# Kernel tuning notes

Measured on AMD Instinct MI355X. Metric: run time of the kernel, lower is better.

The kernel has to match this reference:

```python
import jax, jax.numpy as jnp
import numpy as np
import math

EMB = 768
B, S = 8, 2048

def setup_inputs() -> dict:
    key = jax.random.key(0)
    ks = jax.random.split(key, 6)
    q = jax.random.normal(ks[0], (B, S, EMB), dtype=jnp.float32)
    k = jax.random.normal(ks[1], (B, S, EMB), dtype=jnp.float32)
    v = jax.random.normal(ks[2], (B, S, EMB), dtype=jnp.float32)
    mask = jax.random.randint(ks[3], (B, S, S), 0, 2, dtype=jnp.int32)
    # nn.Linear(emb, emb): weight [out, in], bias [out]
    bound = 1.0 / math.sqrt(EMB)
    W = jax.random.uniform(ks[4], (EMB, EMB), minval=-bound, maxval=bound, dtype=jnp.float32)
    b = jax.random.uniform(ks[5], (EMB,), minval=-bound, maxval=bound, dtype=jnp.float32)
    return {"q": q, "k": k, "v": v, "mask": mask, "W": W, "b": b}

def reference(q, k, v, mask, W, b):
    # shared linear projection (torch Linear: x @ W^T + b)
    qp = jnp.einsum('bse,oe->bso', q, W) + b
    kp = jnp.einsum('bse,oe->bso', k, W) + b
    vp = jnp.einsum('bse,oe->bso', v, W) + b
    scores = jnp.einsum('bqe,bke->bqk', qp, kp) / math.sqrt(EMB)  # [B,S,S]
    scores = jnp.where(mask == 1, -jnp.inf, scores)
    attn = jax.nn.softmax(scores, axis=-1)
    return jnp.einsum('bqk,bke->bqe', attn, vp)
```

## Files before the change

### kernel.cpp

```cpp
#include <hip/hip_runtime.h>
#include <hip/hip_bf16.h>
#include <stdint.h>

#define B_ 8
#define S_ 2048
#define E_ 768

typedef __attribute__((ext_vector_type(4))) float f32x4;
typedef __attribute__((ext_vector_type(8))) short bf16x8;


__device__ __forceinline__ unsigned pk2bf(float x, float y) {
  unsigned r;
  asm("v_cvt_pk_bf16_f32 %0, %1, %2" : "=v"(r) : "v"(x), "v"(y));
  return r;
}

__device__ __forceinline__ void gll16(const void* g, void* l) {
  __builtin_amdgcn_global_load_lds((const __attribute__((address_space(1))) void*)g,
                                   (__attribute__((address_space(3))) void*)l, 16, 0, 0);
}

__device__ __forceinline__ void gemm128(const char* __restrict__ Ab,
                                        const char* __restrict__ Bb,
                                        int ldA, int ldB, int NT,
                                        unsigned short* As, unsigned short* Bs,
                                        int tid, int wm, int wn, int lane,
                                        f32x4 (&acc)[4][4]) {
  unsigned sA[2], sB[2], lin2[2];
#pragma unroll
  for (int i = 0; i < 2; ++i) {
    const unsigned lin = (unsigned)i * 4096u + (unsigned)tid * 16u;
    const unsigned row = lin >> 6, ch = (lin >> 4) & 3u;
    const unsigned sw = (ch ^ ((row >> 1) & 3u)) << 4;
    sA[i] = row * (unsigned)ldA + sw;
    sB[i] = row * (unsigned)ldB + sw;
    lin2[i] = lin;
  }
  unsigned aoff[4], boff[4];
#pragma unroll
  for (int m = 0; m < 4; ++m) {
    unsigned row = (unsigned)(wm * 64 + m * 16 + (lane & 15));
    aoff[m] = row * 64 + ((((unsigned)lane >> 4) ^ ((row >> 1) & 3u)) << 4);
    row = (unsigned)(wn * 64 + m * 16 + (lane & 15));
    boff[m] = row * 64 + ((((unsigned)lane >> 4) ^ ((row >> 1) & 3u)) << 4);
  }
#pragma unroll
  for (int i = 0; i < 2; ++i) {
    gll16(Ab + sA[i], (char*)As + lin2[i]);
    gll16(Bb + sB[i], (char*)Bs + lin2[i]);
  }
  asm volatile("s_waitcnt vmcnt(0)" ::: "memory");
  __builtin_amdgcn_s_barrier();
  __builtin_amdgcn_sched_barrier(0);
  for (int kt = 0; kt < NT; ++kt) {
    const char* Ac = (const char*)As + (kt & 1) * 8192;
    const char* Bc = (const char*)Bs + (kt & 1) * 8192;
    char* An = (char*)As + ((kt + 1) & 1) * 8192;
    char* Bn = (char*)Bs + ((kt + 1) & 1) * 8192;
    if (kt + 1 < NT) {
      const size_t ko = (size_t)(kt + 1) * 64;
#pragma unroll
      for (int i = 0; i < 2; ++i) {
        gll16(Ab + sA[i] + ko, An + lin2[i]);
        gll16(Bb + sB[i] + ko, Bn + lin2[i]);
      }
    }
    bf16x8 af[4], bf[4];
#pragma unroll
    for (int m = 0; m < 4; ++m) af[m] = *reinterpret_cast<const bf16x8*>(Ac + aoff[m]);
#pragma unroll
    for (int n = 0; n < 4; ++n) bf[n] = *reinterpret_cast<const bf16x8*>(Bc + boff[n]);
    asm volatile("s_waitcnt lgkmcnt(0)" ::: "memory");
    __builtin_amdgcn_sched_barrier(0);
    __builtin_amdgcn_s_setprio(1);
#pragma unroll
    for (int m = 0; m < 4; ++m)
#pragma unroll
      for (int n = 0; n < 4; ++n)
        acc[m][n] = __builtin_amdgcn_mfma_f32_16x16x32_bf16(af[m], bf[n], acc[m][n], 0, 0, 0);
    __builtin_amdgcn_s_setprio(0);
    if (kt + 1 < NT) {
      asm volatile("s_waitcnt vmcnt(0)" ::: "memory");
      __builtin_amdgcn_s_barrier();
      __builtin_amdgcn_sched_barrier(0);
    }
  }
}

__global__ __launch_bounds__(256) void k_cvt(const float* __restrict__ q,
                                             const float* __restrict__ k,
                                             const float* __restrict__ v,
                                             const float* __restrict__ W,
                                             const int* __restrict__ mask,
                                             unsigned short* __restrict__ qb,
                                             unsigned short* __restrict__ kb,
                                             unsigned short* __restrict__ vb,
                                             unsigned short* __restrict__ Wb,
                                             unsigned long long* __restrict__ mwords) {
  const int y = blockIdx.y;
  if (y == 3) {
    const int nchunks = B_ * S_ * (S_ / 256);
    const int lane = threadIdx.x & 63;
    const int wave = (blockIdx.x * 256 + threadIdx.x) >> 6;
    const int nw = gridDim.x * 4;
    int c = wave;
    for (; c + 3 * nw < nchunks; c += 4 * nw) {
      int4 v0 = *reinterpret_cast<const int4*>(&mask[(size_t)c * 256 + lane * 4]);
      int4 v1 = *reinterpret_cast<const int4*>(&mask[(size_t)(c + nw) * 256 + lane * 4]);
      int4 v2 = *reinterpret_cast<const int4*>(&mask[(size_t)(c + 2 * nw) * 256 + lane * 4]);
      int4 v3 = *reinterpret_cast<const int4*>(&mask[(size_t)(c + 3 * nw) * 256 + lane * 4]);
      unsigned long long a0 = __ballot(v0.x == 1), a1 = __ballot(v0.y == 1);
      unsigned long long a2 = __ballot(v0.z == 1), a3 = __ballot(v0.w == 1);
      unsigned long long b0 = __ballot(v1.x == 1), b1 = __ballot(v1.y == 1);
      unsigned long long b2 = __ballot(v1.z == 1), b3 = __ballot(v1.w == 1);
      unsigned long long c0 = __ballot(v2.x == 1), c1 = __ballot(v2.y == 1);
      unsigned long long c2 = __ballot(v2.z == 1), c3 = __ballot(v2.w == 1);
      unsigned long long d0 = __ballot(v3.x == 1), d1 = __ballot(v3.y == 1);
      unsigned long long d2 = __ballot(v3.z == 1), d3 = __ballot(v3.w == 1);
      if (lane == 0) {
        *reinterpret_cast<ulonglong2*>(&mwords[(size_t)c * 4]) = make_ulonglong2(a0, a1);
        *reinterpret_cast<ulonglong2*>(&mwords[(size_t)c * 4 + 2]) = make_ulonglong2(a2, a3);
        *reinterpret_cast<ulonglong2*>(&mwords[(size_t)(c + nw) * 4]) = make_ulonglong2(b0, b1);
        *reinterpret_cast<ulonglong2*>(&mwords[(size_t)(c + nw) * 4 + 2]) = make_ulonglong2(b2, b3);
        *reinterpret_cast<ulonglong2*>(&mwords[(size_t)(c + 2 * nw) * 4]) = make_ulonglong2(c0, c1);
        *reinterpret_cast<ulonglong2*>(&mwords[(size_t)(c + 2 * nw) * 4 + 2]) = make_ulonglong2(c2, c3);
        *reinterpret_cast<ulonglong2*>(&mwords[(size_t)(c + 3 * nw) * 4]) = make_ulonglong2(d0, d1);
        *reinterpret_cast<ulonglong2*>(&mwords[(size_t)(c + 3 * nw) * 4 + 2]) = make_ulonglong2(d2, d3);
      }
    }
    for (; c < nchunks; c += nw) {
      int4 v0 = *reinterpret_cast<const int4*>(&mask[(size_t)c * 256 + lane * 4]);
      unsigned long long a0 = __ballot(v0.x == 1), a1 = __ballot(v0.y == 1);
      unsigned long long a2 = __ballot(v0.z == 1), a3 = __ballot(v0.w == 1);
      if (lane == 0) {
        *reinterpret_cast<ulonglong2*>(&mwords[(size_t)c * 4]) = make_ulonglong2(a0, a1);
        *reinterpret_cast<ulonglong2*>(&mwords[(size_t)c * 4 + 2]) = make_ulonglong2(a2, a3);
      }
    }
    return;
  }
  if (y == 4) {
    if (blockIdx.x < 288) {
      const int i0 = blockIdx.x * 512 + threadIdx.x;
      const float4* s4 = reinterpret_cast<const float4*>(W);
      uint2* d2 = reinterpret_cast<uint2*>(Wb);
      float4 f0 = s4[i0];
      float4 f1 = s4[i0 + 256];
      d2[i0]       = make_uint2(pk2bf(f0.x, f0.y), pk2bf(f0.z, f0.w));
      d2[i0 + 256] = make_uint2(pk2bf(f1.x, f1.y), pk2bf(f1.z, f1.w));
    }
    return;
  }
  const float* src = (y == 0) ? q : (y == 1) ? k : v;
  unsigned short* dst = (y == 0) ? qb : (y == 1) ? kb : vb;
  const int i0 = blockIdx.x * 512 + threadIdx.x;
  const float4* s4 = reinterpret_cast<const float4*>(src);
  uint2* d2 = reinterpret_cast<uint2*>(dst);
  float4 f0 = s4[i0];
  float4 f1 = s4[i0 + 256];
  d2[i0]       = make_uint2(pk2bf(f0.x, f0.y), pk2bf(f0.z, f0.w));
  d2[i0 + 256] = make_uint2(pk2bf(f1.x, f1.y), pk2bf(f1.z, f1.w));
}

__global__ __launch_bounds__(256, 4) void k_projb(const unsigned short* __restrict__ Xb,
                                                  const unsigned short* __restrict__ Wb,
                                                  const float* __restrict__ bias,
                                                  unsigned short* __restrict__ qp,
                                                  unsigned short* __restrict__ kp,
                                                  unsigned short* __restrict__ vpT) {
  __shared__ __attribute__((aligned(16))) unsigned short SM[16896];
  unsigned short* As = SM;
  unsigned short* Bs = SM + 8192;
  const int tid = threadIdx.x, lane = tid & 63, wid = tid >> 6;
  const int wm = wid >> 1, wn = wid & 1;
  const int id = blockIdx.x;
  const int swz = (id & 7) * 288 + (id >> 3);
  const int z = swz / 768;
  const int rem = swz - z * 768;
  const int r0 = (rem / 6) * 128, c0 = (rem % 6) * 128;
  const unsigned short* X = Xb + (size_t)z * (B_ * S_ * E_);

  f32x4 acc[4][4] = {};
  gemm128((const char*)(X + (size_t)r0 * E_), (const char*)(Wb + (size_t)c0 * E_),
          E_ * 2, E_ * 2, E_ / 32, As, Bs, tid, wm, wn, lane, acc);

  float bcol[4];
#pragma unroll
  for (int n = 0; n < 4; ++n) bcol[n] = bias[c0 + wn * 64 + n * 16 + (lane & 15)];

  if (z == 2) {
    __syncthreads();
#pragma unroll
    for (int m = 0; m < 4; ++m)
#pragma unroll
      for (int r = 0; r < 4; ++r) {
        const int row = wm * 64 + m * 16 + (lane >> 4) * 4 + r;
#pragma unroll
        for (int n = 0; n < 4; ++n) {
          const int col = wn * 64 + n * 16 + (lane & 15);
          SM[col * 132 + row] = (unsigned short)pk2bf(acc[m][n][r] + bcol[n], 0.f);
        }
      }
    __syncthreads();
    const int b = r0 >> 11;
    const int s0 = r0 & 2047;
#pragma unroll
    for (int i = 0; i < 16; ++i) {
      const int f = i * 256 + tid;
      const int e = f >> 5, su = f & 31;
      uint2 val = *reinterpret_cast<const uint2*>(&SM[e * 132 + su * 4]);
      *reinterpret_cast<uint2*>(&vpT[((size_t)b * E_ + c0 + e) * S_ + s0 + su * 4]) = val;
    }
    return;
  }

  unsigned short* O = (z == 0) ? qp : kp;
#pragma unroll
  for (int m = 0; m < 4; ++m)
#pragma unroll
    for (int r = 0; r < 4; ++r) {
      const int row = r0 + wm * 64 + m * 16 + (lane >> 4) * 4 + r;
#pragma unroll
      for (int n = 0; n < 4; ++n) {
        const int col = c0 + wn * 64 + n * 16 + (lane & 15);
        O[(size_t)row * E_ + col] = (unsigned short)pk2bf(acc[m][n][r] + bcol[n], 0.f);
      }
    }
}

__global__ __launch_bounds__(256, 4) void k_scores(const unsigned short* __restrict__ qp,
                                                   const unsigned short* __restrict__ kp,
                                                   const unsigned long long* __restrict__ mwords,
                                                   unsigned short* __restrict__ P,
                                                   float* __restrict__ rowsum) {
  __shared__ __attribute__((aligned(16))) unsigned short SM[16384];
  unsigned short* As = SM;
  unsigned short* Bs = SM + 8192;
  float* rlds = (float*)SM;
  const int tid = threadIdx.x, lane = tid & 63, wid = tid >> 6;
  const int wm = wid >> 1, wn = wid & 1;
  const int id = blockIdx.x;
  const int swz = (id & 7) * 256 + (id >> 3);
  const int b = swz >> 8;
  const int qt = (swz >> 4) & 15, yt = swz & 15;
  f32x4 acc[4][4] = {};
  gemm128((const char*)(qp + ((size_t)b * S_ + qt * 128) * E_),
          (const char*)(kp + ((size_t)b * S_ + yt * 128) * E_),
          E_ * 2, E_ * 2, E_ / 32, As, Bs, tid, wm, wn, lane, acc);
  __syncthreads();

  const float SC = (float)(1.4426950408889634 / 27.712812921102035);
#pragma unroll
  for (int m = 0; m < 4; ++m)
#pragma unroll
    for (int r = 0; r < 4; ++r) {
      const int rloc = wm * 64 + m * 16 + (lane >> 4) * 4 + r;
      const int grow = qt * 128 + rloc;
      const size_t rowoff = ((size_t)b * S_ + grow) * S_;
      const unsigned long long mw =
          mwords[(((size_t)b * S_ + grow) * 8 + (yt >> 1)) * 4 + (lane & 3)];
      const int shb = (yt & 1) * 32 + wn * 16 + ((lane & 15) >> 2);
      const int cbase = yt * 128 + wn * 64 + (lane & 15);
      float radd = 0.f;
#pragma unroll
      for (int n = 0; n < 4; ++n) {
        float pv = ((mw >> (shb + n * 4)) & 1ull)
                       ? 0.f
                       : __builtin_amdgcn_exp2f(acc[m][n][r] * SC);
        radd += pv;
        P[rowoff + cbase + n * 16] = (unsigned short)pk2bf(pv, 0.f);
      }
      float vsum = radd;
      vsum += __shfl_xor(vsum, 1);
      vsum += __shfl_xor(vsum, 2);
      vsum += __shfl_xor(vsum, 4);
      vsum += __shfl_xor(vsum, 8);
      if ((lane & 15) == 0) rlds[rloc * 2 + wn] = vsum;
    }
  __syncthreads();
  if (tid < 128) {
    rowsum[(size_t)yt * (B_ * S_) + (size_t)b * S_ + qt * 128 + tid] =
        rlds[tid * 2] + rlds[tid * 2 + 1];
  }
}

__global__ __launch_bounds__(256) void k_invrs(const float* __restrict__ rowsum,
                                               float* __restrict__ inv_rs) {
  int i = blockIdx.x * 256 + threadIdx.x;
  float t = 0.f;
#pragma unroll
  for (int g = 0; g < 16; ++g) t += rowsum[(size_t)g * (B_ * S_) + i];
  inv_rs[i] = 1.0f / t;
}

__global__ __launch_bounds__(256, 4) void k_pv(const unsigned short* __restrict__ P,
                                               const unsigned short* __restrict__ vpT,
                                               const float* __restrict__ inv_rs,
                                               float* __restrict__ out) {
  __shared__ __attribute__((aligned(16))) unsigned short SM[16384];
  unsigned short* As = SM;
  unsigned short* Bs = SM + 8192;
  const int tid = threadIdx.x, lane = tid & 63, wid = tid >> 6;
  const int wm = wid >> 1, wn = wid & 1;
  const int id = blockIdx.x;
  const int swz = (id & 7) * 96 + (id >> 3);
  const int b = swz / 96;
  const int rem = swz - b * 96;
  const int mt = rem / 6, et = rem % 6;
  f32x4 acc[4][4] = {};
  gemm128((const char*)(P + ((size_t)b * S_ + mt * 128) * S_),
          (const char*)(vpT + ((size_t)b * E_ + et * 128) * S_),
          S_ * 2, S_ * 2, S_ / 32, As, Bs, tid, wm, wn, lane, acc);

#pragma unroll
  for (int m = 0; m < 4; ++m)
#pragma unroll
    for (int r = 0; r < 4; ++r) {
      const int grow = mt * 128 + wm * 64 + m * 16 + (lane >> 4) * 4 + r;
      const float inv = inv_rs[b * S_ + grow];
#pragma unroll
      for (int n = 0; n < 4; ++n) {
        const int col = et * 128 + wn * 64 + n * 16 + (lane & 15);
        out[((size_t)b * S_ + grow) * E_ + col] = acc[m][n][r] * inv;
      }
    }
}

extern "C" void kernel_launch(void* const* d_in, const int* in_sizes, int n_in,
                              void* d_out, int out_size, void* d_ws, size_t ws_size,
                              hipStream_t stream) {
  const float* q = (const float*)d_in[0];
  const float* k = (const float*)d_in[1];
  const float* v = (const float*)d_in[2];
  const int* mask = (const int*)d_in[3];
  const float* W = (const float*)d_in[4];
  const float* bias = (const float*)d_in[5];
  float* out = (float*)d_out;
  char* ws = (char*)d_ws;

  unsigned short* qb = (unsigned short*)(ws + 0);
  unsigned short* kb = (unsigned short*)(ws + 25165824);
  unsigned short* vb = (unsigned short*)(ws + 50331648);
  unsigned short* Wb = (unsigned short*)(ws + 75497472);
  unsigned short* qp = (unsigned short*)(ws + 76677120);
  unsigned short* kp = (unsigned short*)(ws + 101842944);
  unsigned short* vpT = (unsigned short*)(ws + 127008768);
  unsigned short* P = (unsigned short*)(ws + 0);
  float* rowsum = (float*)(ws + 75497472);
  float* inv_rs = (float*)(ws + 76546048);
  unsigned long long* mwords =
      (unsigned long long*)((char*)d_out + 25165824);
  (void)in_sizes; (void)n_in; (void)out_size; (void)ws_size;

  dim3 blk(256, 1, 1);
  k_cvt<<<dim3(6144, 5, 1), blk, 0, stream>>>(q, k, v, W, mask, qb, kb, vb, Wb, mwords);
  k_projb<<<dim3(2304, 1, 1), blk, 0, stream>>>(qb, Wb, bias, qp, kp, vpT);
  k_scores<<<dim3(2048, 1, 1), blk, 0, stream>>>(qp, kp, mwords, P, rowsum);
  k_invrs<<<dim3(64, 1, 1), blk, 0, stream>>>(rowsum, inv_rs);
  k_pv<<<dim3(768, 1, 1), blk, 0, stream>>>(P, vpT, inv_rs, out);
}
```

Baseline: 287.2 us.

## Fuse fp32-to-bf16 activation conversion into projection GEMM A-operand loads

The projection GEMM now reads q/k/v directly as fp32 from global memory into registers, converts them to bf16 in-kernel, and writes the result into swizzled LDS. This removes the separate conversion pass, along with the bf16 copies it wrote to and read back from the workspace. The mask packing and W conversion are split into their own kernels. The trade-off is that the GEMM now reads twice the A bytes and its A operand goes through a register-staged path instead of direct global-to-LDS loads, which may reduce overlap in the main loop.

```diff
diff --git a/kernel.cpp b/kernel.cpp
--- a/kernel.cpp
+++ b/kernel.cpp
@@ -88,82 +88,153 @@
   }
 }
 
-__global__ __launch_bounds__(256) void k_cvt(const float* __restrict__ q,
-                                             const float* __restrict__ k,
-                                             const float* __restrict__ v,
-                                             const float* __restrict__ W,
-                                             const int* __restrict__ mask,
-                                             unsigned short* __restrict__ qb,
-                                             unsigned short* __restrict__ kb,
-                                             unsigned short* __restrict__ vb,
-                                             unsigned short* __restrict__ Wb,
-                                             unsigned long long* __restrict__ mwords) {
-  const int y = blockIdx.y;
-  if (y == 3) {
-    const int nchunks = B_ * S_ * (S_ / 256);
-    const int lane = threadIdx.x & 63;
-    const int wave = (blockIdx.x * 256 + threadIdx.x) >> 6;
-    const int nw = gridDim.x * 4;
-    int c = wave;
-    for (; c + 3 * nw < nchunks; c += 4 * nw) {
-      int4 v0 = *reinterpret_cast<const int4*>(&mask[(size_t)c * 256 + lane * 4]);
-      int4 v1 = *reinterpret_cast<const int4*>(&mask[(size_t)(c + nw) * 256 + lane * 4]);
-      int4 v2 = *reinterpret_cast<const int4*>(&mask[(size_t)(c + 2 * nw) * 256 + lane * 4]);
-      int4 v3 = *reinterpret_cast<const int4*>(&mask[(size_t)(c + 3 * nw) * 256 + lane * 4]);
-      unsigned long long a0 = __ballot(v0.x == 1), a1 = __ballot(v0.y == 1);
-      unsigned long long a2 = __ballot(v0.z == 1), a3 = __ballot(v0.w == 1);
-      unsigned long long b0 = __ballot(v1.x == 1), b1 = __ballot(v1.y == 1);
-      unsigned long long b2 = __ballot(v1.z == 1), b3 = __ballot(v1.w == 1);
-      unsigned long long c0 = __ballot(v2.x == 1), c1 = __ballot(v2.y == 1);
-      unsigned long long c2 = __ballot(v2.z == 1), c3 = __ballot(v2.w == 1);
-      unsigned long long d0 = __ballot(v3.x == 1), d1 = __ballot(v3.y == 1);
-      unsigned long long d2 = __ballot(v3.z == 1), d3 = __ballot(v3.w == 1);
-      if (lane == 0) {
-        *reinterpret_cast<ulonglong2*>(&mwords[(size_t)c * 4]) = make_ulonglong2(a0, a1);
-        *reinterpret_cast<ulonglong2*>(&mwords[(size_t)c * 4 + 2]) = make_ulonglong2(a2, a3);
-        *reinterpret_cast<ulonglong2*>(&mwords[(size_t)(c + nw) * 4]) = make_ulonglong2(b0, b1);
-        *reinterpret_cast<ulonglong2*>(&mwords[(size_t)(c + nw) * 4 + 2]) = make_ulonglong2(b2, b3);
-        *reinterpret_cast<ulonglong2*>(&mwords[(size_t)(c + 2 * nw) * 4]) = make_ulonglong2(c0, c1);
-        *reinterpret_cast<ulonglong2*>(&mwords[(size_t)(c + 2 * nw) * 4 + 2]) = make_ulonglong2(c2, c3);
-        *reinterpret_cast<ulonglong2*>(&mwords[(size_t)(c + 3 * nw) * 4]) = make_ulonglong2(d0, d1);
-        *reinterpret_cast<ulonglong2*>(&mwords[(size_t)(c + 3 * nw) * 4 + 2]) = make_ulonglong2(d2, d3);
-      }
-    }
-    for (; c < nchunks; c += nw) {
-      int4 v0 = *reinterpret_cast<const int4*>(&mask[(size_t)c * 256 + lane * 4]);
-      unsigned long long a0 = __ballot(v0.x == 1), a1 = __ballot(v0.y == 1);
-      unsigned long long a2 = __ballot(v0.z == 1), a3 = __ballot(v0.w == 1);
-      if (lane == 0) {
-        *reinterpret_cast<ulonglong2*>(&mwords[(size_t)c * 4]) = make_ulonglong2(a0, a1);
-        *reinterpret_cast<ulonglong2*>(&mwords[(size_t)c * 4 + 2]) = make_ulonglong2(a2, a3);
-      }
-    }
-    return;
-  }
-  if (y == 4) {
-    if (blockIdx.x < 288) {
-      const int i0 = blockIdx.x * 512 + threadIdx.x;
-      const float4* s4 = reinterpret_cast<const float4*>(W);
-      uint2* d2 = reinterpret_cast<uint2*>(Wb);
-      float4 f0 = s4[i0];
-      float4 f1 = s4[i0 + 256];
-      d2[i0]       = make_uint2(pk2bf(f0.x, f0.y), pk2bf(f0.z, f0.w));
-      d2[i0 + 256] = make_uint2(pk2bf(f1.x, f1.y), pk2bf(f1.z, f1.w));
-    }
-    return;
-  }
-  const float* src = (y == 0) ? q : (y == 1) ? k : v;
-  unsigned short* dst = (y == 0) ? qb : (y == 1) ? kb : vb;
+__device__ __forceinline__ void gemm128_f32A(const char* __restrict__ Af0, int ldAf,
+                                             const char* __restrict__ Bb, int ldB, int NT,
+                                             unsigned short* As, unsigned short* Bs,
+                                             int tid, int wm, int wn, int lane,
+                                             f32x4 (&acc)[4][4]) {
+  unsigned sB[2], lin2[2];
+#pragma unroll
+  for (int i = 0; i < 2; ++i) {
+    const unsigned lin = (unsigned)i * 4096u + (unsigned)tid * 16u;
+    const unsigned row = lin >> 6, ch = (lin >> 4) & 3u;
+    const unsigned sw = (ch ^ ((row >> 1) & 3u)) << 4;
+    sB[i] = row * (unsigned)ldB + sw;
+    lin2[i] = lin;
+  }
+  const int arow = tid >> 1;
+  const int ahalf = tid & 1;
+  const char* Afb = Af0 + (size_t)arow * ldAf + (size_t)ahalf * 64;
+  unsigned awoff[2];
+#pragma unroll
+  for (int c = 0; c < 2; ++c) {
+    const unsigned chunk = (unsigned)(ahalf * 2 + c);
+    awoff[c] = (unsigned)arow * 64 + ((chunk ^ (((unsigned)arow >> 1) & 3u)) << 4);
+  }
+  unsigned aoff[4], boff[4];
+#pragma unroll
+  for (int m = 0; m < 4; ++m) {
+    unsigned row = (unsigned)(wm * 64 + m * 16 + (lane & 15));
+    aoff[m] = row * 64 + ((((unsigned)lane >> 4) ^ ((row >> 1) & 3u)) << 4);
+    row = (unsigned)(wn * 64 + m * 16 + (lane & 15));
+    boff[m] = row * 64 + ((((unsigned)lane >> 4) ^ ((row >> 1) & 3u)) << 4);
+  }
+  float4 fa[4];
+#pragma unroll
+  for (int i = 0; i < 4; ++i) fa[i] = *reinterpret_cast<const float4*>(Afb + i * 16);
+#pragma unroll
+  for (int i = 0; i < 2; ++i) gll16(Bb + sB[i], (char*)Bs + lin2[i]);
+  asm volatile("s_waitcnt vmcnt(0)" ::: "memory");
+  {
+    uint4 w0 = make_uint4(pk2bf(fa[0].x, fa[0].y), pk2bf(fa[0].z, fa[0].w),
+                          pk2bf(fa[1].x, fa[1].y), pk2bf(fa[1].z, fa[1].w));
+    uint4 w1 = make_uint4(pk2bf(fa[2].x, fa[2].y), pk2bf(fa[2].z, fa[2].w),
+                          pk2bf(fa[3].x, fa[3].y), pk2bf(fa[3].z, fa[3].w));
+    *reinterpret_cast<uint4*>((char*)As + awoff[0]) = w0;
+    *reinterpret_cast<uint4*>((char*)As + awoff[1]) = w1;
+  }
+  asm volatile("s_waitcnt lgkmcnt(0)" ::: "memory");
+  __builtin_amdgcn_s_barrier();
+  __builtin_amdgcn_sched_barrier(0);
+  for (int kt = 0; kt < NT; ++kt) {
+    const char* Ac = (const char*)As + (kt & 1) * 8192;
+    const char* Bc = (const char*)Bs + (kt & 1) * 8192;
+    char* An = (char*)As + ((kt + 1) & 1) * 8192;
+    char* Bn = (char*)Bs + ((kt + 1) & 1) * 8192;
+    if (kt + 1 < NT) {
+      const size_t ko = (size_t)(kt + 1) * 128;
+#pragma unroll
+      for (int i = 0; i < 4; ++i)
+        fa[i] = *reinterpret_cast<const float4*>(Afb + ko + i * 16);
+#pragma unroll
+      for (int i = 0; i < 2; ++i)
+        gll16(Bb + sB[i] + (size_t)(kt + 1) * 64, Bn + lin2[i]);
+    }
+    bf16x8 af[4], bf[4];
+#pragma unroll
+    for (int m = 0; m < 4; ++m) af[m] = *reinterpret_cast<const bf16x8*>(Ac + aoff[m]);
+#pragma unroll
+    for (int n = 0; n < 4; ++n) bf[n] = *reinterpret_cast<const bf16x8*>(Bc + boff[n]);
+    asm volatile("s_waitcnt lgkmcnt(0)" ::: "memory");
+    __builtin_amdgcn_sched_barrier(0);
+    __builtin_amdgcn_s_setprio(1);
+#pragma unroll
+    for (int m = 0; m < 4; ++m)
+#pragma unroll
+      for (int n = 0; n < 4; ++n)
+        acc[m][n] = __builtin_amdgcn_mfma_f32_16x16x32_bf16(af[m], bf[n], acc[m][n], 0, 0, 0);
+    __builtin_amdgcn_s_setprio(0);
+    if (kt + 1 < NT) {
+      asm volatile("s_waitcnt vmcnt(0)" ::: "memory");
+      uint4 w0 = make_uint4(pk2bf(fa[0].x, fa[0].y), pk2bf(fa[0].z, fa[0].w),
+                            pk2bf(fa[1].x, fa[1].y), pk2bf(fa[1].z, fa[1].w));
+      uint4 w1 = make_uint4(pk2bf(fa[2].x, fa[2].y), pk2bf(fa[2].z, fa[2].w),
+                            pk2bf(fa[3].x, fa[3].y), pk2bf(fa[3].z, fa[3].w));
+      *reinterpret_cast<uint4*>(An + awoff[0]) = w0;
+      *reinterpret_cast<uint4*>(An + awoff[1]) = w1;
+      asm volatile("s_waitcnt lgkmcnt(0)" ::: "memory");
+      __builtin_amdgcn_s_barrier();
+      __builtin_amdgcn_sched_barrier(0);
+    }
+  }
+}
+
+__global__ __launch_bounds__(256) void k_cvtW(const float* __restrict__ W,
+                                              unsigned short* __restrict__ Wb) {
   const int i0 = blockIdx.x * 512 + threadIdx.x;
-  const float4* s4 = reinterpret_cast<const float4*>(src);
-  uint2* d2 = reinterpret_cast<uint2*>(dst);
+  const float4* s4 = reinterpret_cast<const float4*>(W);
+  uint2* d2 = reinterpret_cast<uint2*>(Wb);
   float4 f0 = s4[i0];
   float4 f1 = s4[i0 + 256];
   d2[i0]       = make_uint2(pk2bf(f0.x, f0.y), pk2bf(f0.z, f0.w));
   d2[i0 + 256] = make_uint2(pk2bf(f1.x, f1.y), pk2bf(f1.z, f1.w));
 }
 
-__global__ __launch_bounds__(256, 4) void k_projb(const unsigned short* __restrict__ Xb,
+__global__ __launch_bounds__(256) void k_pack(const int* __restrict__ mask,
+                                              unsigned long long* __restrict__ mwords) {
+  const int nchunks = B_ * S_ * (S_ / 256);
+  const int lane = threadIdx.x & 63;
+  const int wave = (blockIdx.x * 256 + threadIdx.x) >> 6;
+  const int nw = gridDim.x * 4;
+  int c = wave;
+  for (; c + 3 * nw < nchunks; c += 4 * nw) {
+    int4 v0 = *reinterpret_cast<const int4*>(&mask[(size_t)c * 256 + lane * 4]);
+    int4 v1 = *reinterpret_cast<const int4*>(&mask[(size_t)(c + nw) * 256 + lane * 4]);
+    int4 v2 = *reinterpret_cast<const int4*>(&mask[(size_t)(c + 2 * nw) * 256 + lane * 4]);
+    int4 v3 = *reinterpret_cast<const int4*>(&mask[(size_t)(c + 3 * nw) * 256 + lane * 4]);
+    unsigned long long a0 = __ballot(v0.x == 1), a1 = __ballot(v0.y == 1);
+    unsigned long long a2 = __ballot(v0.z == 1), a3 = __ballot(v0.w == 1);
+    unsigned long long b0 = __ballot(v1.x == 1), b1 = __ballot(v1.y == 1);
+    unsigned long long b2 = __ballot(v1.z == 1), b3 = __ballot(v1.w == 1);
+    unsigned long long c0 = __ballot(v2.x == 1), c1 = __ballot(v2.y == 1);
+    unsigned long long c2 = __ballot(v2.z == 1), c3 = __ballot(v2.w == 1);
+    unsigned long long d0 = __ballot(v3.x == 1), d1 = __ballot(v3.y == 1);
+    unsigned long long d2 = __ballot(v3.z == 1), d3 = __ballot(v3.w == 1);
+    if (lane == 0) {
+      *reinterpret_cast<ulonglong2*>(&mwords[(size_t)c * 4]) = make_ulonglong2(a0, a1);
+      *reinterpret_cast<ulonglong2*>(&mwords[(size_t)c * 4 + 2]) = make_ulonglong2(a2, a3);
+      *reinterpret_cast<ulonglong2*>(&mwords[(size_t)(c + nw) * 4]) = make_ulonglong2(b0, b1);
+      *reinterpret_cast<ulonglong2*>(&mwords[(size_t)(c + nw) * 4 + 2]) = make_ulonglong2(b2, b3);
+      *reinterpret_cast<ulonglong2*>(&mwords[(size_t)(c + 2 * nw) * 4]) = make_ulonglong2(c0, c1);
+      *reinterpret_cast<ulonglong2*>(&mwords[(size_t)(c + 2 * nw) * 4 + 2]) = make_ulonglong2(c2, c3);
+      *reinterpret_cast<ulonglong2*>(&mwords[(size_t)(c + 3 * nw) * 4]) = make_ulonglong2(d0, d1);
+      *reinterpret_cast<ulonglong2*>(&mwords[(size_t)(c + 3 * nw) * 4 + 2]) = make_ulonglong2(d2, d3);
+    }
+  }
+  for (; c < nchunks; c += nw) {
+    int4 v0 = *reinterpret_cast<const int4*>(&mask[(size_t)c * 256 + lane * 4]);
+    unsigned long long a0 = __ballot(v0.x == 1), a1 = __ballot(v0.y == 1);
+    unsigned long long a2 = __ballot(v0.z == 1), a3 = __ballot(v0.w == 1);
+    if (lane == 0) {
+      *reinterpret_cast<ulonglong2*>(&mwords[(size_t)c * 4]) = make_ulonglong2(a0, a1);
+      *reinterpret_cast<ulonglong2*>(&mwords[(size_t)c * 4 + 2]) = make_ulonglong2(a2, a3);
+    }
+  }
+}
+
+__global__ __launch_bounds__(256, 4) void k_projb(const float* __restrict__ q,
+                                                  const float* __restrict__ k,
+                                                  const float* __restrict__ v,
                                                   const unsigned short* __restrict__ Wb,
                                                   const float* __restrict__ bias,
                                                   unsigned short* __restrict__ qp,
@@ -179,11 +250,12 @@
   const int z = swz / 768;
   const int rem = swz - z * 768;
   const int r0 = (rem / 6) * 128, c0 = (rem % 6) * 128;
-  const unsigned short* X = Xb + (size_t)z * (B_ * S_ * E_);
+  const float* X = (z == 0) ? q : (z == 1) ? k : v;
 
   f32x4 acc[4][4] = {};
-  gemm128((const char*)(X + (size_t)r0 * E_), (const char*)(Wb + (size_t)c0 * E_),
-          E_ * 2, E_ * 2, E_ / 32, As, Bs, tid, wm, wn, lane, acc);
+  gemm128_f32A((const char*)(X + (size_t)r0 * E_), E_ * 4,
+               (const char*)(Wb + (size_t)c0 * E_), E_ * 2, E_ / 32,
+               As, Bs, tid, wm, wn, lane, acc);
 
   float bcol[4];
 #pragma unroll
@@ -339,9 +411,6 @@
   float* out = (float*)d_out;
   char* ws = (char*)d_ws;
 
-  unsigned short* qb = (unsigned short*)(ws + 0);
-  unsigned short* kb = (unsigned short*)(ws + 25165824);
-  unsigned short* vb = (unsigned short*)(ws + 50331648);
   unsigned short* Wb = (unsigned short*)(ws + 75497472);
   unsigned short* qp = (unsigned short*)(ws + 76677120);
   unsigned short* kp = (unsigned short*)(ws + 101842944);
@@ -354,8 +423,9 @@
   (void)in_sizes; (void)n_in; (void)out_size; (void)ws_size;
 
   dim3 blk(256, 1, 1);
-  k_cvt<<<dim3(6144, 5, 1), blk, 0, stream>>>(q, k, v, W, mask, qb, kb, vb, Wb, mwords);
-  k_projb<<<dim3(2304, 1, 1), blk, 0, stream>>>(qb, Wb, bias, qp, kp, vpT);
+  k_cvtW<<<dim3(288, 1, 1), blk, 0, stream>>>(W, Wb);
+  k_pack<<<dim3(6144, 1, 1), blk, 0, stream>>>(mask, mwords);
+  k_projb<<<dim3(2304, 1, 1), blk, 0, stream>>>(q, k, v, Wb, bias, qp, kp, vpT);
   k_scores<<<dim3(2048, 1, 1), blk, 0, stream>>>(qp, kp, mwords, P, rowsum);
   k_invrs<<<dim3(64, 1, 1), blk, 0, stream>>>(rowsum, inv_rs);
   k_pv<<<dim3(768, 1, 1), blk, 0, stream>>>(P, vpT, inv_rs, out);
```

Result: slower. 294.3 us (+2.5%).

## Split fused conversion kernel and use 128x64 tiles for PV GEMM

Applied to the files above, without the earlier changes.

Splits the fused multi-purpose conversion kernel into separate q/k/v cast, W cast and mask bit-pack kernels, with the mask pack launched on 2048 blocks instead of 6144. Adds a 128x64 tiled GEMM helper and switches the P·V kernel to it. The helper doubles the block count to 1536, cuts LDS per block, and raises launch bounds to 6 blocks per CU for better occupancy and load balance. In exchange, each block reuses less data per tile, so global traffic for P rises, and the extra launches add overhead.

```diff
diff --git a/kernel.cpp b/kernel.cpp
--- a/kernel.cpp
+++ b/kernel.cpp
@@ -88,72 +88,88 @@
   }
 }
 
-__global__ __launch_bounds__(256) void k_cvt(const float* __restrict__ q,
-                                             const float* __restrict__ k,
-                                             const float* __restrict__ v,
-                                             const float* __restrict__ W,
-                                             const int* __restrict__ mask,
-                                             unsigned short* __restrict__ qb,
-                                             unsigned short* __restrict__ kb,
-                                             unsigned short* __restrict__ vb,
-                                             unsigned short* __restrict__ Wb,
-                                             unsigned long long* __restrict__ mwords) {
-  const int y = blockIdx.y;
-  if (y == 3) {
-    const int nchunks = B_ * S_ * (S_ / 256);
-    const int lane = threadIdx.x & 63;
-    const int wave = (blockIdx.x * 256 + threadIdx.x) >> 6;
-    const int nw = gridDim.x * 4;
-    int c = wave;
-    for (; c + 3 * nw < nchunks; c += 4 * nw) {
-      int4 v0 = *reinterpret_cast<const int4*>(&mask[(size_t)c * 256 + lane * 4]);
-      int4 v1 = *reinterpret_cast<const int4*>(&mask[(size_t)(c + nw) * 256 + lane * 4]);
-      int4 v2 = *reinterpret_cast<const int4*>(&mask[(size_t)(c + 2 * nw) * 256 + lane * 4]);
-      int4 v3 = *reinterpret_cast<const int4*>(&mask[(size_t)(c + 3 * nw) * 256 + lane * 4]);
-      unsigned long long a0 = __ballot(v0.x == 1), a1 = __ballot(v0.y == 1);
-      unsigned long long a2 = __ballot(v0.z == 1), a3 = __ballot(v0.w == 1);
-      unsigned long long b0 = __ballot(v1.x == 1), b1 = __ballot(v1.y == 1);
-      unsigned long long b2 = __ballot(v1.z == 1), b3 = __ballot(v1.w == 1);
-      unsigned long long c0 = __ballot(v2.x == 1), c1 = __ballot(v2.y == 1);
-      unsigned long long c2 = __ballot(v2.z == 1), c3 = __ballot(v2.w == 1);
-      unsigned long long d0 = __ballot(v3.x == 1), d1 = __ballot(v3.y == 1);
-      unsigned long long d2 = __ballot(v3.z == 1), d3 = __ballot(v3.w == 1);
-      if (lane == 0) {
-        *reinterpret_cast<ulonglong2*>(&mwords[(size_t)c * 4]) = make_ulonglong2(a0, a1);
-        *reinterpret_cast<ulonglong2*>(&mwords[(size_t)c * 4 + 2]) = make_ulonglong2(a2, a3);
-        *reinterpret_cast<ulonglong2*>(&mwords[(size_t)(c + nw) * 4]) = make_ulonglong2(b0, b1);
-        *reinterpret_cast<ulonglong2*>(&mwords[(size_t)(c + nw) * 4 + 2]) = make_ulonglong2(b2, b3);
-        *reinterpret_cast<ulonglong2*>(&mwords[(size_t)(c + 2 * nw) * 4]) = make_ulonglong2(c0, c1);
-        *reinterpret_cast<ulonglong2*>(&mwords[(size_t)(c + 2 * nw) * 4 + 2]) = make_ulonglong2(c2, c3);
-        *reinterpret_cast<ulonglong2*>(&mwords[(size_t)(c + 3 * nw) * 4]) = make_ulonglong2(d0, d1);
-        *reinterpret_cast<ulonglong2*>(&mwords[(size_t)(c + 3 * nw) * 4 + 2]) = make_ulonglong2(d2, d3);
-      }
-    }
-    for (; c < nchunks; c += nw) {
-      int4 v0 = *reinterpret_cast<const int4*>(&mask[(size_t)c * 256 + lane * 4]);
-      unsigned long long a0 = __ballot(v0.x == 1), a1 = __ballot(v0.y == 1);
-      unsigned long long a2 = __ballot(v0.z == 1), a3 = __ballot(v0.w == 1);
-      if (lane == 0) {
-        *reinterpret_cast<ulonglong2*>(&mwords[(size_t)c * 4]) = make_ulonglong2(a0, a1);
-        *reinterpret_cast<ulonglong2*>(&mwords[(size_t)c * 4 + 2]) = make_ulonglong2(a2, a3);
-      }
-    }
-    return;
-  }
-  if (y == 4) {
-    if (blockIdx.x < 288) {
-      const int i0 = blockIdx.x * 512 + threadIdx.x;
-      const float4* s4 = reinterpret_cast<const float4*>(W);
-      uint2* d2 = reinterpret_cast<uint2*>(Wb);
-      float4 f0 = s4[i0];
-      float4 f1 = s4[i0 + 256];
-      d2[i0]       = make_uint2(pk2bf(f0.x, f0.y), pk2bf(f0.z, f0.w));
-      d2[i0 + 256] = make_uint2(pk2bf(f1.x, f1.y), pk2bf(f1.z, f1.w));
-    }
-    return;
-  }
-  const float* src = (y == 0) ? q : (y == 1) ? k : v;
-  unsigned short* dst = (y == 0) ? qb : (y == 1) ? kb : vb;
+__device__ __forceinline__ void gemm128x64(const char* __restrict__ Ab,
+                                           const char* __restrict__ Bb,
+                                           int ldA, int ldB, int NT,
+                                           unsigned short* As, unsigned short* Bs,
+                                           int tid, int wm, int wn, int lane,
+                                           f32x4 (&acc)[4][2]) {
+  unsigned sA[2], lin2[2];
+#pragma unroll
+  for (int i = 0; i < 2; ++i) {
+    const unsigned lin = (unsigned)i * 4096u + (unsigned)tid * 16u;
+    const unsigned row = lin >> 6, ch = (lin >> 4) & 3u;
+    const unsigned sw = (ch ^ ((row >> 1) & 3u)) << 4;
+    sA[i] = row * (unsigned)ldA + sw;
+    lin2[i] = lin;
+  }
+  unsigned sB0, linB;
+  {
+    const unsigned lin = (unsigned)tid * 16u;
+    const unsigned row = lin >> 6, ch = (lin >> 4) & 3u;
+    const unsigned sw = (ch ^ ((row >> 1) & 3u)) << 4;
+    sB0 = row * (unsigned)ldB + sw;
+    linB = lin;
+  }
+  unsigned aoff[4], boff[2];
+#pragma unroll
+  for (int m = 0; m < 4; ++m) {
+    unsigned row = (unsigned)(wm * 64 + m * 16 + (lane & 15));
+    aoff[m] = row * 64 + ((((unsigned)lane >> 4) ^ ((row >> 1) & 3u)) << 4);
+  }
+#pragma unroll
+  for (int j = 0; j < 2; ++j) {
+    unsigned row = (unsigned)(wn * 32 + j * 16 + (lane & 15));
+    boff[j] = row * 64 + ((((unsigned)lane >> 4) ^ ((row >> 1) & 3u)) << 4);
+  }
+#pragma unroll
+  for (int i = 0; i < 2; ++i) gll16(Ab + sA[i], (char*)As + lin2[i]);
+  gll16(Bb + sB0, (char*)Bs + linB);
+  asm volatile("s_waitcnt vmcnt(0)" ::: "memory");
+  __builtin_amdgcn_s_barrier();
+  __builtin_amdgcn_sched_barrier(0);
+  for (int kt = 0; kt < NT; ++kt) {
+    const char* Ac = (const char*)As + (kt & 1) * 8192;
+    const char* Bc = (const char*)Bs + (kt & 1) * 4096;
+    char* An = (char*)As + ((kt + 1) & 1) * 8192;
+    char* Bn = (char*)Bs + ((kt + 1) & 1) * 4096;
+    if (kt + 1 < NT) {
+      const size_t ko = (size_t)(kt + 1) * 64;
+#pragma unroll
+      for (int i = 0; i < 2; ++i) gll16(Ab + sA[i] + ko, An + lin2[i]);
+      gll16(Bb + sB0 + ko, Bn + linB);
+    }
+    bf16x8 af[4], bf[2];
+#pragma unroll
+    for (int m = 0; m < 4; ++m) af[m] = *reinterpret_cast<const bf16x8*>(Ac + aoff[m]);
+#pragma unroll
+    for (int j = 0; j < 2; ++j) bf[j] = *reinterpret_cast<const bf16x8*>(Bc + boff[j]);
+    asm volatile("s_waitcnt lgkmcnt(0)" ::: "memory");
+    __builtin_amdgcn_sched_barrier(0);
+    __builtin_amdgcn_s_setprio(1);
+#pragma unroll
+    for (int m = 0; m < 4; ++m)
+#pragma unroll
+      for (int j = 0; j < 2; ++j)
+        acc[m][j] = __builtin_amdgcn_mfma_f32_16x16x32_bf16(af[m], bf[j], acc[m][j], 0, 0, 0);
+    __builtin_amdgcn_s_setprio(0);
+    if (kt + 1 < NT) {
+      asm volatile("s_waitcnt vmcnt(0)" ::: "memory");
+      __builtin_amdgcn_s_barrier();
+      __builtin_amdgcn_sched_barrier(0);
+    }
+  }
+}
+
+__global__ __launch_bounds__(256) void k_cvt3(const float* __restrict__ q,
+                                              const float* __restrict__ k,
+                                              const float* __restrict__ v,
+                                              unsigned short* __restrict__ qb,
+                                              unsigned short* __restrict__ kb,
+                                              unsigned short* __restrict__ vb) {
+  const int z = blockIdx.y;
+  const float* src = (z == 0) ? q : (z == 1) ? k : v;
+  unsigned short* dst = (z == 0) ? qb : (z == 1) ? kb : vb;
   const int i0 = blockIdx.x * 512 + threadIdx.x;
   const float4* s4 = reinterpret_cast<const float4*>(src);
   uint2* d2 = reinterpret_cast<uint2*>(dst);
@@ -161,6 +177,59 @@
   float4 f1 = s4[i0 + 256];
   d2[i0]       = make_uint2(pk2bf(f0.x, f0.y), pk2bf(f0.z, f0.w));
   d2[i0 + 256] = make_uint2(pk2bf(f1.x, f1.y), pk2bf(f1.z, f1.w));
+}
+
+__global__ __launch_bounds__(256) void k_cvtW(const float* __restrict__ W,
+                                              unsigned short* __restrict__ Wb) {
+  const int i0 = blockIdx.x * 512 + threadIdx.x;
+  const float4* s4 = reinterpret_cast<const float4*>(W);
+  uint2* d2 = reinterpret_cast<uint2*>(Wb);
+  float4 f0 = s4[i0];
+  float4 f1 = s4[i0 + 256];
+  d2[i0]       = make_uint2(pk2bf(f0.x, f0.y), pk2bf(f0.z, f0.w));
+  d2[i0 + 256] = make_uint2(pk2bf(f1.x, f1.y), pk2bf(f1.z, f1.w));
+}
+
+__global__ __launch_bounds__(256) void k_pack(const int* __restrict__ mask,
+                                              unsigned long long* __restrict__ mwords) {
+  const int nchunks = B_ * S_ * (S_ / 256);
+  const int lane = threadIdx.x & 63;
+  const int wave = (blockIdx.x * 256 + threadIdx.x) >> 6;
+  const int nw = gridDim.x * 4;
+  int c = wave;
+  for (; c + 3 * nw < nchunks; c += 4 * nw) {
+    int4 v0 = *reinterpret_cast<const int4*>(&mask[(size_t)c * 256 + lane * 4]);
+    int4 v1 = *reinterpret_cast<const int4*>(&mask[(size_t)(c + nw) * 256 + lane * 4]);
+    int4 v2 = *reinterpret_cast<const int4*>(&mask[(size_t)(c + 2 * nw) * 256 + lane * 4]);
+    int4 v3 = *reinterpret_cast<const int4*>(&mask[(size_t)(c + 3 * nw) * 256 + lane * 4]);
+    unsigned long long a0 = __ballot(v0.x == 1), a1 = __ballot(v0.y == 1);
+    unsigned long long a2 = __ballot(v0.z == 1), a3 = __ballot(v0.w == 1);
+    unsigned long long b0 = __ballot(v1.x == 1), b1 = __ballot(v1.y == 1);
+    unsigned long long b2 = __ballot(v1.z == 1), b3 = __ballot(v1.w == 1);
+    unsigned long long c0 = __ballot(v2.x == 1), c1 = __ballot(v2.y == 1);
+    unsigned long long c2 = __ballot(v2.z == 1), c3 = __ballot(v2.w == 1);
+    unsigned long long d0 = __ballot(v3.x == 1), d1 = __ballot(v3.y == 1);
+    unsigned long long d2 = __ballot(v3.z == 1), d3 = __ballot(v3.w == 1);
+    if (lane == 0) {
+      *reinterpret_cast<ulonglong2*>(&mwords[(size_t)c * 4]) = make_ulonglong2(a0, a1);
+      *reinterpret_cast<ulonglong2*>(&mwords[(size_t)c * 4 + 2]) = make_ulonglong2(a2, a3);
+      *reinterpret_cast<ulonglong2*>(&mwords[(size_t)(c + nw) * 4]) = make_ulonglong2(b0, b1);
+      *reinterpret_cast<ulonglong2*>(&mwords[(size_t)(c + nw) * 4 + 2]) = make_ulonglong2(b2, b3);
+      *reinterpret_cast<ulonglong2*>(&mwords[(size_t)(c + 2 * nw) * 4]) = make_ulonglong2(c0, c1);
+      *reinterpret_cast<ulonglong2*>(&mwords[(size_t)(c + 2 * nw) * 4 + 2]) = make_ulonglong2(c2, c3);
+      *reinterpret_cast<ulonglong2*>(&mwords[(size_t)(c + 3 * nw) * 4]) = make_ulonglong2(d0, d1);
+      *reinterpret_cast<ulonglong2*>(&mwords[(size_t)(c + 3 * nw) * 4 + 2]) = make_ulonglong2(d2, d3);
+    }
+  }
+  for (; c < nchunks; c += nw) {
+    int4 v0 = *reinterpret_cast<const int4*>(&mask[(size_t)c * 256 + lane * 4]);
+    unsigned long long a0 = __ballot(v0.x == 1), a1 = __ballot(v0.y == 1);
+    unsigned long long a2 = __ballot(v0.z == 1), a3 = __ballot(v0.w == 1);
+    if (lane == 0) {
+      *reinterpret_cast<ulonglong2*>(&mwords[(size_t)c * 4]) = make_ulonglong2(a0, a1);
+      *reinterpret_cast<ulonglong2*>(&mwords[(size_t)c * 4 + 2]) = make_ulonglong2(a2, a3);
+    }
+  }
 }
 
 __global__ __launch_bounds__(256, 4) void k_projb(const unsigned short* __restrict__ Xb,
@@ -294,24 +363,24 @@
   inv_rs[i] = 1.0f / t;
 }
 
-__global__ __launch_bounds__(256, 4) void k_pv(const unsigned short* __restrict__ P,
+__global__ __launch_bounds__(256, 6) void k_pv(const unsigned short* __restrict__ P,
                                                const unsigned short* __restrict__ vpT,
                                                const float* __restrict__ inv_rs,
                                                float* __restrict__ out) {
-  __shared__ __attribute__((aligned(16))) unsigned short SM[16384];
+  __shared__ __attribute__((aligned(16))) unsigned short SM[12288];
   unsigned short* As = SM;
   unsigned short* Bs = SM + 8192;
   const int tid = threadIdx.x, lane = tid & 63, wid = tid >> 6;
   const int wm = wid >> 1, wn = wid & 1;
   const int id = blockIdx.x;
-  const int swz = (id & 7) * 96 + (id >> 3);
-  const int b = swz / 96;
-  const int rem = swz - b * 96;
-  const int mt = rem / 6, et = rem % 6;
-  f32x4 acc[4][4] = {};
-  gemm128((const char*)(P + ((size_t)b * S_ + mt * 128) * S_),
-          (const char*)(vpT + ((size_t)b * E_ + et * 128) * S_),
-          S_ * 2, S_ * 2, S_ / 32, As, Bs, tid, wm, wn, lane, acc);
+  const int swz = (id & 7) * 192 + (id >> 3);
+  const int b = swz / 192;
+  const int rem = swz - b * 192;
+  const int mt = rem / 12, et = rem % 12;
+  f32x4 acc[4][2] = {};
+  gemm128x64((const char*)(P + ((size_t)b * S_ + mt * 128) * S_),
+             (const char*)(vpT + ((size_t)b * E_ + et * 64) * S_),
+             S_ * 2, S_ * 2, S_ / 32, As, Bs, tid, wm, wn, lane, acc);
 
 #pragma unroll
   for (int m = 0; m < 4; ++m)
@@ -320,9 +389,9 @@
       const int grow = mt * 128 + wm * 64 + m * 16 + (lane >> 4) * 4 + r;
       const float inv = inv_rs[b * S_ + grow];
 #pragma unroll
-      for (int n = 0; n < 4; ++n) {
-        const int col = et * 128 + wn * 64 + n * 16 + (lane & 15);
-        out[((size_t)b * S_ + grow) * E_ + col] = acc[m][n][r] * inv;
+      for (int j = 0; j < 2; ++j) {
+        const int col = et * 64 + wn * 32 + j * 16 + (lane & 15);
+        out[((size_t)b * S_ + grow) * E_ + col] = acc[m][j][r] * inv;
       }
     }
 }
@@ -354,9 +423,11 @@
   (void)in_sizes; (void)n_in; (void)out_size; (void)ws_size;
 
   dim3 blk(256, 1, 1);
-  k_cvt<<<dim3(6144, 5, 1), blk, 0, stream>>>(q, k, v, W, mask, qb, kb, vb, Wb, mwords);
+  k_cvt3<<<dim3(6144, 3, 1), blk, 0, stream>>>(q, k, v, qb, kb, vb);
+  k_cvtW<<<dim3(288, 1, 1), blk, 0, stream>>>(W, Wb);
+  k_pack<<<dim3(2048, 1, 1), blk, 0, stream>>>(mask, mwords);
   k_projb<<<dim3(2304, 1, 1), blk, 0, stream>>>(qb, Wb, bias, qp, kp, vpT);
   k_scores<<<dim3(2048, 1, 1), blk, 0, stream>>>(qp, kp, mwords, P, rowsum);
   k_invrs<<<dim3(64, 1, 1), blk, 0, stream>>>(rowsum, inv_rs);
-  k_pv<<<dim3(768, 1, 1), blk, 0, stream>>>(P, vpT, inv_rs, out);
-}
+  k_pv<<<dim3(1536, 1, 1), blk, 0, stream>>>(P, vpT, inv_rs, out);
+}
```

Result: slower. 312.0 us (+8.6%).
